# Kernel optimization log

Hardware: AMD Instinct MI355X
Metric: run time of the kernel (lower is better)

Reference implementation:

```python
import jax, jax.numpy as jnp
import numpy as np


def setup_inputs() -> dict:
    key = jax.random.key(0)
    k1, k2, k3 = jax.random.split(key, 3)
    B, A, P, Cm, S, C, G = 2, 512, 8, 6, 4, 256, 8
    # per-scale (H, W) for each of the 6 cameras (same pyramid per camera)
    shapes = np.array([[64, 176], [32, 88], [16, 44], [8, 22]], np.int32)  # [S,2]
    spatial_shape = jnp.asarray(np.tile(shapes[None], (Cm, 1, 1)))  # [Cm,S,2]
    sizes = shapes[:, 0] * shapes[:, 1]  # rows per scale
    starts = np.concatenate([[0], np.cumsum(np.tile(sizes, Cm))])[:-1].reshape(Cm, S).astype(np.int32)
    N = int(sizes.sum() * Cm)  # 89760 flattened feature rows
    mc_ms_feat = jax.random.normal(k1, (B, N, C), jnp.float32)
    sampling_location = jax.random.uniform(k2, (B, A, P, Cm, 2), jnp.float32)
    w = jax.random.uniform(k3, (B, A, P, Cm, S, G), jnp.float32)
    weights = w / jnp.sum(w, axis=(2, 3, 4), keepdims=True)  # normalized over pts/cams/scales
    return {
        "mc_ms_feat": mc_ms_feat,
        "spatial_shape": spatial_shape,
        "scale_start_index": jnp.asarray(starts),
        "sampling_location": sampling_location,
        "weights": weights,
    }


def reference(mc_ms_feat, spatial_shape, scale_start_index, sampling_location, weights):
    B, N, C = mc_ms_feat.shape
    _, A, P, Cm, _ = sampling_location.shape
    S = spatial_shape.shape[1]
    G = weights.shape[-1]
    Hi = spatial_shape[..., 0]  # [Cm,S] int32
    Wi = spatial_shape[..., 1]
    Hf = Hi.astype(mc_ms_feat.dtype)
    Wf = Wi.astype(mc_ms_feat.dtype)
    # pixel-space coords per (b,a,p,cam,scale); align_corners=False convention
    x = sampling_location[..., 0][..., None] * Wf - 0.5  # [B,A,P,Cm,S]
    y = sampling_location[..., 1][..., None] * Hf - 0.5
    x0 = jnp.floor(x)
    y0 = jnp.floor(y)
    x0i = x0.astype(jnp.int32)
    y0i = y0.astype(jnp.int32)
    wx1 = x - x0
    wy1 = y - y0
    batch_ix = jnp.arange(B)[:, None]

    def corner(ix, iy, cw):
        valid = (ix >= 0) & (ix < Wi) & (iy >= 0) & (iy < Hi)
        idx = scale_start_index + jnp.clip(iy, 0, Hi - 1) * Wi + jnp.clip(ix, 0, Wi - 1)
        f = mc_ms_feat[batch_ix, idx.reshape(B, -1)]  # [B, A*P*Cm*S, C]
        cw = jnp.where(valid, cw, 0.0).reshape(B, -1, 1)
        return f * cw

    val = (corner(x0i, y0i, (1.0 - wx1) * (1.0 - wy1))
           + corner(x0i + 1, y0i, wx1 * (1.0 - wy1))
           + corner(x0i, y0i + 1, (1.0 - wx1) * wy1)
           + corner(x0i + 1, y0i + 1, wx1 * wy1))
    # channel groups: C -> (G, D); weight each group, reduce pts/cams/scales
    val = val.reshape(B, A, P, Cm, S, G, C // G)
    out = jnp.einsum('bapcsgd,bapcsg->bagd', val, weights)
    return out.reshape(B, A, C)
```

## Files before the change

### kernel.cpp

```cpp
#include <hip/hip_runtime.h>
#include <hip/hip_fp16.h>

constexpr int B  = 2;
constexpr int A  = 512;
constexpr int P  = 8;
constexpr int CM = 6;
constexpr int SC = 4;
constexpr int C  = 256;
constexpr int G  = 8;
constexpr int NCOMBO = P * CM * SC;
constexpr int NFEAT  = 89760;
constexpr int COMBOS_PER_WAVE = NCOMBO / 4;
constexpr int NGRP = COMBOS_PER_WAVE / 2;

__global__ __launch_bounds__(256)
void convert_fp16_kernel(const float* __restrict__ in,
                         uint2* __restrict__ out,
                         int n4) {
  const float4* in4 = (const float4*)in;
  int i = blockIdx.x * 256 + threadIdx.x;
  const int stride = gridDim.x * 256;
  for (; i < n4; i += stride) {
    const float4 v = in4[i];
    union { __half2 h; unsigned u; } a, b;
    a.h = __floats2half2_rn(v.x, v.y);
    b.h = __floats2half2_rn(v.z, v.w);
    uint2 q; q.x = a.u; q.y = b.u;
    out[i] = q;
  }
}

__global__ __launch_bounds__(256, 4)
void deform_agg_kernel(const uint2* __restrict__ feat16,
                       const int*   __restrict__ spatial,
                       const int*   __restrict__ scale_start,
                       const float* __restrict__ samp_loc,
                       const float* __restrict__ weights,
                       float*       __restrict__ out) {
  __shared__ int    s_idx[NCOMBO][4];
  __shared__ float  s_cw[NCOMBO][4];
  __shared__ float  s_wg[NCOMBO * G];
  __shared__ float4 s_red[4][64];

  const int tid = threadIdx.x;
  const int ba  = blockIdx.x;
  const int b   = ba >> 9;

  if (tid < NCOMBO) {
    const int p   = tid / (CM * SC);
    const int cam = (tid / SC) % CM;
    const int s   = tid & (SC - 1);
    const float* lp = samp_loc + ((size_t)(ba * P + p) * CM + cam) * 2;
    const float lx = lp[0];
    const float ly = lp[1];
    const int H  = spatial[(cam * SC + s) * 2 + 0];
    const int W  = spatial[(cam * SC + s) * 2 + 1];
    const int st = scale_start[cam * SC + s];

    const float x = lx * (float)W - 0.5f;
    const float y = ly * (float)H - 0.5f;
    const float x0f = floorf(x), y0f = floorf(y);
    const int   ix0 = (int)x0f,  iy0 = (int)y0f;
    const float wx1 = x - x0f,   wy1 = y - y0f;
    const float wx[2] = {1.f - wx1, wx1};
    const float wy[2] = {1.f - wy1, wy1};
    const int   ix[2] = {ix0, ix0 + 1};
    const int   iy[2] = {iy0, iy0 + 1};
#pragma unroll
    for (int cyi = 0; cyi < 2; ++cyi) {
#pragma unroll
      for (int cxi = 0; cxi < 2; ++cxi) {
        const int k  = cyi * 2 + cxi;
        const int cx = ix[cxi], cy = iy[cyi];
        const bool valid = (cx >= 0) && (cx < W) && (cy >= 0) && (cy < H);
        const int ccx = min(max(cx, 0), W - 1);
        const int ccy = min(max(cy, 0), H - 1);
        s_idx[tid][k] = (st + ccy * W + ccx) * (C / 4);
        s_cw[tid][k]  = valid ? wx[cxi] * wy[cyi] : 0.f;
      }
    }
  }
  {
    const float* wbase = weights + (size_t)ba * NCOMBO * G;
    for (int i = tid; i < NCOMBO * G; i += 256) s_wg[i] = wbase[i];
  }
  __syncthreads();

  const int wid  = tid >> 6;
  const int lane = tid & 63;
  const int g    = lane >> 3;
  const uint2* fb = feat16 + (size_t)b * NFEAT * (C / 4);

  float4 acc = {0.f, 0.f, 0.f, 0.f};
  const int c0 = wid * COMBOS_PER_WAVE;

  auto load_grp = [&](int grp, uint2* f, float* cw) {
#pragma unroll
    for (int j = 0; j < 2; ++j) {
      const int c = c0 + grp * 2 + j;
      const float w = s_wg[c * G + g];
#pragma unroll
      for (int k = 0; k < 4; ++k) {
        cw[j * 4 + k] = s_cw[c][k] * w;
        f[j * 4 + k]  = fb[s_idx[c][k] + lane];
      }
    }
  };
  auto consume = [&](const uint2* f, const float* cw) {
#pragma unroll
    for (int j = 0; j < 8; ++j) {
      const __half2 h0 = *reinterpret_cast<const __half2*>(&f[j].x);
      const __half2 h1 = *reinterpret_cast<const __half2*>(&f[j].y);
      const float2 v01 = __half22float2(h0);
      const float2 v23 = __half22float2(h1);
      acc.x = fmaf(v01.x, cw[j], acc.x);
      acc.y = fmaf(v01.y, cw[j], acc.y);
      acc.z = fmaf(v23.x, cw[j], acc.z);
      acc.w = fmaf(v23.y, cw[j], acc.w);
    }
  };

  uint2 fA[8], fB[8];
  float cwA[8], cwB[8];
  load_grp(0, fA, cwA);
#pragma unroll
  for (int it = 0; it < NGRP - 1; ++it) {
    if ((it & 1) == 0) {
      load_grp(it + 1, fB, cwB);
      consume(fA, cwA);
    } else {
      load_grp(it + 1, fA, cwA);
      consume(fB, cwB);
    }
  }
  consume(fB, cwB);

  s_red[wid][lane] = acc;
  __syncthreads();

  if (wid == 0) {
    const float4 r0 = s_red[0][lane];
    const float4 r1 = s_red[1][lane];
    const float4 r2 = s_red[2][lane];
    const float4 r3 = s_red[3][lane];
    float4 t;
    t.x = (r0.x + r1.x) + (r2.x + r3.x);
    t.y = (r0.y + r1.y) + (r2.y + r3.y);
    t.z = (r0.z + r1.z) + (r2.z + r3.z);
    t.w = (r0.w + r1.w) + (r2.w + r3.w);
    ((float4*)out)[(size_t)ba * (C / 4) + lane] = t;
  }
}

extern "C" void kernel_launch(void* const* d_in, const int* in_sizes, int n_in,
                              void* d_out, int out_size, void* d_ws, size_t ws_size,
                              hipStream_t stream) {
  const float* feat        = (const float*)d_in[0];
  const int*   spatial     = (const int*)d_in[1];
  const int*   scale_start = (const int*)d_in[2];
  const float* samp_loc    = (const float*)d_in[3];
  const float* weights     = (const float*)d_in[4];
  float*       out         = (float*)d_out;
  uint2*       feat16      = (uint2*)d_ws;

  const int n4 = in_sizes[0] / 4;
  convert_fp16_kernel<<<2048, 256, 0, stream>>>(feat, feat16, n4);
  deform_agg_kernel<<<B * A, 256, 0, stream>>>(feat16, spatial, scale_start,
                                               samp_loc, weights, out);
}
```

Measured before the change: 310.6 us.

## Fetch horizontally adjacent bilinear corners as one contiguous 16-byte load per lane

The x0 and x0+1 corners of each bilinear sample are adjacent rows in the fp16 feature buffer, so a 64-lane wave now reads both with a single contiguous 1 KB span of uint4 loads. The low half-wave covers the left corner and the high half-wave the right, with x-edge cases folded into adjusted corner weights. This halves the number of gather instructions per combo and doubles the bytes per load. In exchange it needs a cross-half shuffle reduction before the block reduction and more careful boundary handling. Reads at the last column can fetch one row past the scale or buffer end, though with zero weight.

```diff
diff --git a/kernel.cpp b/kernel.cpp
--- a/kernel.cpp
+++ b/kernel.cpp
@@ -31,16 +31,16 @@
 }
 
 __global__ __launch_bounds__(256, 4)
-void deform_agg_kernel(const uint2* __restrict__ feat16,
+void deform_agg_kernel(const uint4* __restrict__ feat16,
                        const int*   __restrict__ spatial,
                        const int*   __restrict__ scale_start,
                        const float* __restrict__ samp_loc,
                        const float* __restrict__ weights,
                        float*       __restrict__ out) {
-  __shared__ int    s_idx[NCOMBO][4];
+  __shared__ int    s_idx[NCOMBO][2];
   __shared__ float  s_cw[NCOMBO][4];
   __shared__ float  s_wg[NCOMBO * G];
-  __shared__ float4 s_red[4][64];
+  __shared__ float  s_red[4][32][8];
 
   const int tid = threadIdx.x;
   const int ba  = blockIdx.x;
@@ -62,23 +62,28 @@
     const float x0f = floorf(x), y0f = floorf(y);
     const int   ix0 = (int)x0f,  iy0 = (int)y0f;
     const float wx1 = x - x0f,   wy1 = y - y0f;
-    const float wx[2] = {1.f - wx1, wx1};
-    const float wy[2] = {1.f - wy1, wy1};
-    const int   ix[2] = {ix0, ix0 + 1};
-    const int   iy[2] = {iy0, iy0 + 1};
-#pragma unroll
-    for (int cyi = 0; cyi < 2; ++cyi) {
-#pragma unroll
-      for (int cxi = 0; cxi < 2; ++cxi) {
-        const int k  = cyi * 2 + cxi;
-        const int cx = ix[cxi], cy = iy[cyi];
-        const bool valid = (cx >= 0) && (cx < W) && (cy >= 0) && (cy < H);
-        const int ccx = min(max(cx, 0), W - 1);
-        const int ccy = min(max(cy, 0), H - 1);
-        s_idx[tid][k] = (st + ccy * W + ccx) * (C / 4);
-        s_cw[tid][k]  = valid ? wx[cxi] * wy[cyi] : 0.f;
-      }
+
+    int   bx;
+    float wxlo, wxhi;
+    if (ix0 >= 0 && ix0 < W) {
+      bx = ix0;  wxlo = 1.f - wx1;  wxhi = (ix0 + 1 < W) ? wx1 : 0.f;
+    } else if (ix0 == -1) {
+      bx = 0;    wxlo = wx1;        wxhi = 0.f;
+    } else {
+      bx = (ix0 < 0) ? 0 : (W - 1);  wxlo = 0.f;  wxhi = 0.f;
     }
+    const int   iy1 = iy0 + 1;
+    const float wy0 = (iy0 >= 0 && iy0 < H) ? (1.f - wy1) : 0.f;
+    const float wyb = (iy1 >= 0 && iy1 < H) ? wy1 : 0.f;
+    const int   ry0 = min(max(iy0, 0), H - 1);
+    const int   ry1 = min(max(iy1, 0), H - 1);
+
+    s_idx[tid][0] = (st + ry0 * W + bx) * 32;
+    s_idx[tid][1] = (st + ry1 * W + bx) * 32;
+    s_cw[tid][0]  = wxlo * wy0;
+    s_cw[tid][1]  = wxhi * wy0;
+    s_cw[tid][2]  = wxlo * wyb;
+    s_cw[tid][3]  = wxhi * wyb;
   }
   {
     const float* wbase = weights + (size_t)ba * NCOMBO * G;
@@ -88,40 +93,41 @@
 
   const int wid  = tid >> 6;
   const int lane = tid & 63;
-  const int g    = lane >> 3;
-  const uint2* fb = feat16 + (size_t)b * NFEAT * (C / 4);
+  const int hi   = lane >> 5;
+  const int g    = (lane & 31) >> 2;
+  const uint4* fb = feat16 + (size_t)b * NFEAT * 32;
 
-  float4 acc = {0.f, 0.f, 0.f, 0.f};
+  float acc[8] = {0.f, 0.f, 0.f, 0.f, 0.f, 0.f, 0.f, 0.f};
   const int c0 = wid * COMBOS_PER_WAVE;
 
-  auto load_grp = [&](int grp, uint2* f, float* cw) {
+  auto load_grp = [&](int grp, uint4* f, float* cw) {
 #pragma unroll
-    for (int j = 0; j < 2; ++j) {
-      const int c = c0 + grp * 2 + j;
+    for (int jc = 0; jc < 2; ++jc) {
+      const int c = c0 + grp * 2 + jc;
       const float w = s_wg[c * G + g];
+      cw[jc * 2 + 0] = s_cw[c][hi] * w;
+      cw[jc * 2 + 1] = s_cw[c][2 + hi] * w;
+      f[jc * 2 + 0]  = fb[s_idx[c][0] + lane];
+      f[jc * 2 + 1]  = fb[s_idx[c][1] + lane];
+    }
+  };
+  auto consume = [&](const uint4* f, const float* cw) {
+#pragma unroll
+    for (int j = 0; j < 4; ++j) {
+      const float w = cw[j];
+      const unsigned* q = &f[j].x;
 #pragma unroll
       for (int k = 0; k < 4; ++k) {
-        cw[j * 4 + k] = s_cw[c][k] * w;
-        f[j * 4 + k]  = fb[s_idx[c][k] + lane];
+        const __half2 h = *reinterpret_cast<const __half2*>(&q[k]);
+        const float2 v = __half22float2(h);
+        acc[2 * k + 0] = fmaf(v.x, w, acc[2 * k + 0]);
+        acc[2 * k + 1] = fmaf(v.y, w, acc[2 * k + 1]);
       }
     }
   };
-  auto consume = [&](const uint2* f, const float* cw) {
-#pragma unroll
-    for (int j = 0; j < 8; ++j) {
-      const __half2 h0 = *reinterpret_cast<const __half2*>(&f[j].x);
-      const __half2 h1 = *reinterpret_cast<const __half2*>(&f[j].y);
-      const float2 v01 = __half22float2(h0);
-      const float2 v23 = __half22float2(h1);
-      acc.x = fmaf(v01.x, cw[j], acc.x);
-      acc.y = fmaf(v01.y, cw[j], acc.y);
-      acc.z = fmaf(v23.x, cw[j], acc.z);
-      acc.w = fmaf(v23.y, cw[j], acc.w);
-    }
-  };
 
-  uint2 fA[8], fB[8];
-  float cwA[8], cwB[8];
+  uint4 fA[4], fB[4];
+  float cwA[4], cwB[4];
   load_grp(0, fA, cwA);
 #pragma unroll
   for (int it = 0; it < NGRP - 1; ++it) {
@@ -135,20 +141,19 @@
   }
   consume(fB, cwB);
 
-  s_red[wid][lane] = acc;
+#pragma unroll
+  for (int j = 0; j < 8; ++j) acc[j] += __shfl_xor(acc[j], 32);
+  if (lane < 32) {
+#pragma unroll
+    for (int j = 0; j < 8; ++j) s_red[wid][lane][j] = acc[j];
+  }
   __syncthreads();
 
-  if (wid == 0) {
-    const float4 r0 = s_red[0][lane];
-    const float4 r1 = s_red[1][lane];
-    const float4 r2 = s_red[2][lane];
-    const float4 r3 = s_red[3][lane];
-    float4 t;
-    t.x = (r0.x + r1.x) + (r2.x + r3.x);
-    t.y = (r0.y + r1.y) + (r2.y + r3.y);
-    t.z = (r0.z + r1.z) + (r2.z + r3.z);
-    t.w = (r0.w + r1.w) + (r2.w + r3.w);
-    ((float4*)out)[(size_t)ba * (C / 4) + lane] = t;
+  {
+    const int l8 = tid >> 3, j = tid & 7;
+    const float v = s_red[0][l8][j] + s_red[1][l8][j] +
+                    s_red[2][l8][j] + s_red[3][l8][j];
+    out[(size_t)ba * C + 8 * l8 + j] = v;
   }
 }
 
@@ -165,6 +170,7 @@
 
   const int n4 = in_sizes[0] / 4;
   convert_fp16_kernel<<<2048, 256, 0, stream>>>(feat, feat16, n4);
-  deform_agg_kernel<<<B * A, 256, 0, stream>>>(feat16, spatial, scale_start,
-                                               samp_loc, weights, out);
+  deform_agg_kernel<<<B * A, 256, 0, stream>>>((const uint4*)d_ws, spatial,
+                                               scale_start, samp_loc, weights,
+                                               out);
 }
```

New measurement: 310.8 us. About the same (+0.1%).
